# Kernel tuning notes

Hardware: AMD Instinct MI355X
Metric: run time of the kernel (lower is better)

Reference implementation:

```python
import jax, jax.numpy as jnp
import numpy as np

TOP_K = 2  # active_experts


def setup_inputs() -> dict:
    key = jax.random.key(0)
    k0, k1, k2, k3 = jax.random.split(key, 4)
    B, S, D, E, H = 4, 1024, 2048, 16, 1024
    x = jax.random.normal(k0, (B, S, D), jnp.float32) * 0.02
    Wg = jax.random.normal(k1, (E, D), jnp.float32) * 0.02          # gate: Linear(dim, E, bias=False)
    balance_bias = jnp.zeros((E,), jnp.float32)                      # registered buffer, init zeros
    W1 = jax.random.normal(k2, (E, D, H), jnp.float32) * 0.02        # expert up-proj (no bias)
    W2 = jax.random.normal(k3, (E, H, D), jnp.float32) * 0.02        # expert down-proj (no bias)
    return {"x": x, "Wg": Wg, "balance_bias": balance_bias, "W1": W1, "W2": W2}


def reference(x, Wg, balance_bias, W1, W2):
    B, S, D = x.shape
    E = Wg.shape[0]
    xf = x.reshape(-1, D)                                   # [T, D], T = B*S
    T = xf.shape[0]

    # sigmoid gating with load-balance bias
    gate_logits = xf @ Wg.T                                 # [T, E]
    gate_scores = jax.nn.sigmoid(gate_logits + balance_bias)

    # top-k selection + normalization (matches torch.topk + sum-normalize)
    topk_scores, topk_idx = jax.lax.top_k(gate_scores, TOP_K)
    topk_scores = topk_scores / (topk_scores.sum(-1, keepdims=True) + 1e-6)

    # dense combine weights [T, E]: zero for unselected experts -> identical math
    # to the per-expert masked index_add in the original module
    combine = jnp.zeros((T, E), xf.dtype).at[jnp.arange(T)[:, None], topk_idx].add(topk_scores)

    # per-expert FFN: SiLU(x W1_e) W2_e, weighted-combined across experts
    h = jax.nn.silu(jnp.einsum('td,edh->teh', xf, W1))      # [T, E, H]
    out = jnp.einsum('teh,te,ehd->td', h, combine, W2)      # [T, D]
    return out.reshape(B, S, D)
```

## Files before the change

### kernel.cpp

```cpp
#include <hip/hip_runtime.h>
#include <math.h>

#define T_TOK 4096
#define DDIM  2048
#define HDIM  1024
#define NEXP  16
#define CAP   4096
#define GBM   128
#define GBN   128
#define GBK   64
#define MAX_TILES 80

typedef __attribute__((ext_vector_type(8))) short  short8;
typedef __attribute__((ext_vector_type(4))) float  floatx4;

__device__ __forceinline__ unsigned short f2bf(float f) {
    unsigned int u = __float_as_uint(f);
    u += 0x7fffu + ((u >> 16) & 1u);
    return (unsigned short)(u >> 16);
}
__device__ __forceinline__ float bf2f(unsigned short u) {
    return __uint_as_float((unsigned int)u << 16);
}

__device__ __forceinline__ void gl_lds16(const void* g, void* l) {
    __builtin_amdgcn_global_load_lds(
        (const __attribute__((address_space(1))) unsigned int*)g,
        (__attribute__((address_space(3))) unsigned int*)l,
        16, 0, 0);
}

__global__ __launch_bounds__(256, 4) void prep_kernel(
    const float* __restrict__ x, const float* __restrict__ Wg,
    const float* __restrict__ bias,
    const float* __restrict__ W1, const float* __restrict__ W2,
    unsigned short* __restrict__ W1T, unsigned short* __restrict__ W2T,
    int* __restrict__ counts, int* __restrict__ tok_list,
    int4* __restrict__ tinfo, float2* __restrict__ wcomb,
    unsigned short* __restrict__ xbf)
{
    __shared__ __align__(16) unsigned short Ls[64 * 256];
    int z   = blockIdx.z;
    int bid = blockIdx.x;
    int tid = threadIdx.x;

    if (bid < 128) {
        const float* src; unsigned short* dst; int K, N, kt, nt;
        if (z < NEXP) {
            K = DDIM; N = HDIM;
            src = W1 + (size_t)z * K * N;
            dst = W1T + (size_t)z * (size_t)N * K;
            kt = bid >> 4; nt = bid & 15;
        } else {
            K = HDIM; N = DDIM;
            src = W2 + (size_t)(z - NEXP) * K * N;
            dst = W2T + (size_t)(z - NEXP) * (size_t)N * K;
            kt = bid >> 5; nt = bid & 31;
        }
        int kb = kt * 256, nb = nt * 64;
        int r = tid >> 4;
        int c16 = tid & 15;
        const float* s0 = src + (size_t)kb * N + nb + c16 * 4;

        float4 v[16];
#pragma unroll
        for (int i4 = 0; i4 < 4; ++i4)
#pragma unroll
            for (int i = 0; i < 4; ++i)
                v[i4 * 4 + i] = *(const float4*)(s0 + (size_t)(i4 * 64 + r * 4 + i) * N);

#pragma unroll
        for (int i4 = 0; i4 < 4; ++i4) {
#pragma unroll
            for (int j = 0; j < 4; ++j) {
                unsigned int lo = (unsigned int)f2bf(((const float*)&v[i4 * 4 + 0])[j])
                                | ((unsigned int)f2bf(((const float*)&v[i4 * 4 + 1])[j]) << 16);
                unsigned int hi = (unsigned int)f2bf(((const float*)&v[i4 * 4 + 2])[j])
                                | ((unsigned int)f2bf(((const float*)&v[i4 * 4 + 3])[j]) << 16);
                int n  = c16 * 4 + j;
                int g  = i4 * 16 + r;
                int gp = g ^ (n & 14);
                *(uint2*)&Ls[n * 256 + gp * 4] = make_uint2(lo, hi);
            }
        }
        __syncthreads();
        unsigned short* d0 = dst + (size_t)nb * K + kb;
#pragma unroll
        for (int j = 0; j < 8; ++j) {
            int c = tid + j * 256;
            int n = c >> 5, a = c & 31;
            int sp = (2 * a) ^ (n & 14);
            short8 sv = *(const short8*)&Ls[n * 256 + sp * 4];
            *(short8*)(d0 + (size_t)n * K + a * 8) = sv;
        }
        return;
    }

    int gb   = z * 8 + (bid - 128);
    int wv   = tid >> 6;
    int lane = tid & 63;
    const float4* wg4 = (const float4*)Wg;

    for (int tk = 0; tk < 4; ++tk) {
        int t = gb * 16 + wv * 4 + tk;

        const float4* xp4 = (const float4*)x + (size_t)t * (DDIM / 4);
        ushort4* xbp4 = (ushort4*)(xbf + (size_t)t * DDIM);

        float acc[NEXP];
#pragma unroll
        for (int e = 0; e < NEXP; ++e) acc[e] = 0.f;

        for (int it = 0; it < DDIM / 4 / 64; ++it) {
            int d4 = it * 64 + lane;
            float4 xv = xp4[d4];
            ushort4 xs;
            xs.x = f2bf(xv.x); xs.y = f2bf(xv.y);
            xs.z = f2bf(xv.z); xs.w = f2bf(xv.w);
            xbp4[d4] = xs;
#pragma unroll
            for (int e = 0; e < NEXP; ++e) {
                float4 wvv = wg4[e * (DDIM / 4) + d4];
                acc[e] += xv.x * wvv.x + xv.y * wvv.y + xv.z * wvv.z + xv.w * wvv.w;
            }
        }
#pragma unroll
        for (int e = 0; e < NEXP; ++e) {
            float v = acc[e];
#pragma unroll
            for (int off = 32; off > 0; off >>= 1) v += __shfl_xor(v, off, 64);
            acc[e] = v;
        }
        if (lane == 0) {
            float s[NEXP];
#pragma unroll
            for (int e = 0; e < NEXP; ++e)
                s[e] = 1.f / (1.f + expf(-(acc[e] + bias[e])));
            int i0 = 0;
#pragma unroll
            for (int e = 1; e < NEXP; ++e) if (s[e] > s[i0]) i0 = e;
            int i1 = (i0 == 0) ? 1 : 0;
            for (int e = 0; e < NEXP; ++e)
                if (e != i0 && s[e] > s[i1]) i1 = e;
            float denom = s[i0] + s[i1] + 1e-6f;
            int p0 = atomicAdd(&counts[i0], 1);
            tok_list[i0 * CAP + p0] = t;
            int p1 = atomicAdd(&counts[i1], 1);
            tok_list[i1 * CAP + p1] = t;
            tinfo[t] = make_int4(i0, p0, i1, p1);
            wcomb[t] = make_float2(s[i0] / denom, s[i1] / denom);
        }
    }
}

__global__ void scan_kernel(const int* __restrict__ counts, int* __restrict__ offsets,
                            int* __restrict__ ntiles, int* __restrict__ tile_e,
                            int* __restrict__ tile_mt)
{
    int lane = threadIdx.x;
    int c = (lane < NEXP) ? counts[lane] : 0;
    int incl = c;
#pragma unroll
    for (int d = 1; d < 64; d <<= 1) {
        int v = __shfl_up(incl, d, 64);
        if (lane >= d) incl += v;
    }
    if (lane < NEXP) offsets[lane] = incl - c;
    if (lane == NEXP - 1) offsets[NEXP] = incl;

    int nt_e = (lane < NEXP) ? ((c + GBM - 1) / GBM) : 0;
    int tincl = nt_e;
#pragma unroll
    for (int d = 1; d < 64; d <<= 1) {
        int v = __shfl_up(tincl, d, 64);
        if (lane >= d) tincl += v;
    }
    int tbase = tincl - nt_e;
    if (lane < NEXP) {
        for (int i = 0; i < nt_e; ++i) {
            tile_e[tbase + i]  = lane;
            tile_mt[tbase + i] = i;
        }
        if (lane == NEXP - 1) *ntiles = tbase + nt_e;
    }
}

__global__ __launch_bounds__(256) void up_gemm(
    const unsigned short* __restrict__ xbf, const unsigned short* __restrict__ W1T,
    const int* __restrict__ counts, const int* __restrict__ offsets,
    const int* __restrict__ ntiles, const int* __restrict__ tile_e,
    const int* __restrict__ tile_mt,
    const int* __restrict__ tok_list, unsigned short* __restrict__ hbuf)
{
    int idx = blockIdx.x;
    if (idx >= *ntiles) return;
    int e   = tile_e[idx];
    int mt  = tile_mt[idx];
    int cnt = counts[e];
    int nbase = blockIdx.y * GBN;

    __shared__ __align__(16) unsigned short As[2][GBM * GBK];
    __shared__ __align__(16) unsigned short Bs[2][GBN * GBK];

    int tid = threadIdx.x, lane = tid & 63, wv = tid >> 6;
    int kcL = ((lane & 7) ^ ((lane >> 3) & 7)) * 8;
    int hbase = offsets[e];

    const unsigned short* gA[4];
    const unsigned short* gB[4];
#pragma unroll
    for (int j = 0; j < 4; ++j) {
        int row = wv * 32 + j * 8 + (lane >> 3);
        int m = mt * GBM + row; if (m >= cnt) m = cnt - 1;
        int tok = tok_list[e * CAP + m];
        gA[j] = xbf + (size_t)tok * DDIM + kcL;
        gB[j] = W1T + ((size_t)e * HDIM + nbase + row) * DDIM + kcL;
    }
    int fr = lane & 15, fq = lane >> 4;
    int wm = (wv & 1) * 64, wn = (wv >> 1) * 64;

    floatx4 acc[4][4];
#pragma unroll
    for (int i = 0; i < 4; ++i)
#pragma unroll
        for (int j = 0; j < 4; ++j) acc[i][j] = (floatx4){0.f, 0.f, 0.f, 0.f};

#pragma unroll
    for (int j = 0; j < 4; ++j)
        gl_lds16(gA[j], &As[0][((wv * 4 + j) * 64 + lane) * 8]);
#pragma unroll
    for (int j = 0; j < 4; ++j)
        gl_lds16(gB[j], &Bs[0][((wv * 4 + j) * 64 + lane) * 8]);

    const int NK = DDIM / GBK;
    for (int i = 0; i < NK; ++i) {
        int cur = i & 1, nxt = cur ^ 1;
        __syncthreads();
        if (i + 1 < NK) {
            int k0 = (i + 1) * GBK;
#pragma unroll
            for (int j = 0; j < 4; ++j)
                gl_lds16(gA[j] + k0, &As[nxt][((wv * 4 + j) * 64 + lane) * 8]);
#pragma unroll
            for (int j = 0; j < 4; ++j)
                gl_lds16(gB[j] + k0, &Bs[nxt][((wv * 4 + j) * 64 + lane) * 8]);
        }
#pragma unroll
        for (int ks = 0; ks < 2; ++ks) {
            short8 af[4], bfr[4];
#pragma unroll
            for (int mi = 0; mi < 4; ++mi) {
                int row = wm + mi * 16 + fr;
                int kcs = (ks * 4 + fq) ^ (row & 7);
                af[mi] = *(const short8*)&As[cur][row * GBK + kcs * 8];
            }
#pragma unroll
            for (int ni = 0; ni < 4; ++ni) {
                int row = wn + ni * 16 + fr;
                int kcs = (ks * 4 + fq) ^ (row & 7);
                bfr[ni] = *(const short8*)&Bs[cur][row * GBK + kcs * 8];
            }
#pragma unroll
            for (int mi = 0; mi < 4; ++mi)
#pragma unroll
                for (int ni = 0; ni < 4; ++ni)
                    acc[mi][ni] = __builtin_amdgcn_mfma_f32_16x16x32_bf16(
                        af[mi], bfr[ni], acc[mi][ni], 0, 0, 0);
        }
    }

#pragma unroll
    for (int mi = 0; mi < 4; ++mi) {
#pragma unroll
        for (int r = 0; r < 4; ++r) {
            int row = wm + mi * 16 + fq * 4 + r;
            int m = mt * GBM + row;
            if (m < cnt) {
                size_t ro = (size_t)(hbase + m) * HDIM + nbase + wn;
#pragma unroll
                for (int ni = 0; ni < 4; ++ni) {
                    float u  = acc[mi][ni][r];
                    float hh = u / (1.f + __expf(-u));
                    hbuf[ro + ni * 16 + fr] = f2bf(hh);
                }
            }
        }
    }
}

__global__ __launch_bounds__(256) void down_gemm(
    const unsigned short* __restrict__ hbuf, const unsigned short* __restrict__ W2T,
    const int* __restrict__ counts, const int* __restrict__ offsets,
    const int* __restrict__ ntiles, const int* __restrict__ tile_e,
    const int* __restrict__ tile_mt,
    unsigned short* __restrict__ ybuf)
{
    int idx = blockIdx.x;
    if (idx >= *ntiles) return;
    int e   = tile_e[idx];
    int mt  = tile_mt[idx];
    int cnt = counts[e];
    int nbase = blockIdx.y * GBN;

    __shared__ __align__(16) unsigned short As[2][GBM * GBK];
    __shared__ __align__(16) unsigned short Bs[2][GBN * GBK];

    int tid = threadIdx.x, lane = tid & 63, wv = tid >> 6;
    int kcL = ((lane & 7) ^ ((lane >> 3) & 7)) * 8;
    int hbase = offsets[e];

    const unsigned short* gA[4];
    const unsigned short* gB[4];
#pragma unroll
    for (int j = 0; j < 4; ++j) {
        int row = wv * 32 + j * 8 + (lane >> 3);
        int m = mt * GBM + row; if (m >= cnt) m = cnt - 1;
        gA[j] = hbuf + (size_t)(hbase + m) * HDIM + kcL;
        gB[j] = W2T + ((size_t)e * DDIM + nbase + row) * HDIM + kcL;
    }
    int fr = lane & 15, fq = lane >> 4;
    int wm = (wv & 1) * 64, wn = (wv >> 1) * 64;

    floatx4 acc[4][4];
#pragma unroll
    for (int i = 0; i < 4; ++i)
#pragma unroll
        for (int j = 0; j < 4; ++j) acc[i][j] = (floatx4){0.f, 0.f, 0.f, 0.f};

#pragma unroll
    for (int j = 0; j < 4; ++j)
        gl_lds16(gA[j], &As[0][((wv * 4 + j) * 64 + lane) * 8]);
#pragma unroll
    for (int j = 0; j < 4; ++j)
        gl_lds16(gB[j], &Bs[0][((wv * 4 + j) * 64 + lane) * 8]);

    const int NK = HDIM / GBK;
    for (int i = 0; i < NK; ++i) {
        int cur = i & 1, nxt = cur ^ 1;
        __syncthreads();
        if (i + 1 < NK) {
            int k0 = (i + 1) * GBK;
#pragma unroll
            for (int j = 0; j < 4; ++j)
                gl_lds16(gA[j] + k0, &As[nxt][((wv * 4 + j) * 64 + lane) * 8]);
#pragma unroll
            for (int j = 0; j < 4; ++j)
                gl_lds16(gB[j] + k0, &Bs[nxt][((wv * 4 + j) * 64 + lane) * 8]);
        }
#pragma unroll
        for (int ks = 0; ks < 2; ++ks) {
            short8 af[4], bfr[4];
#pragma unroll
            for (int mi = 0; mi < 4; ++mi) {
                int row = wm + mi * 16 + fr;
                int kcs = (ks * 4 + fq) ^ (row & 7);
                af[mi] = *(const short8*)&As[cur][row * GBK + kcs * 8];
            }
#pragma unroll
            for (int ni = 0; ni < 4; ++ni) {
                int row = wn + ni * 16 + fr;
                int kcs = (ks * 4 + fq) ^ (row & 7);
                bfr[ni] = *(const short8*)&Bs[cur][row * GBK + kcs * 8];
            }
#pragma unroll
            for (int mi = 0; mi < 4; ++mi)
#pragma unroll
                for (int ni = 0; ni < 4; ++ni)
                    acc[mi][ni] = __builtin_amdgcn_mfma_f32_16x16x32_bf16(
                        af[mi], bfr[ni], acc[mi][ni], 0, 0, 0);
        }
    }

#pragma unroll
    for (int mi = 0; mi < 4; ++mi) {
#pragma unroll
        for (int r = 0; r < 4; ++r) {
            int row = wm + mi * 16 + fq * 4 + r;
            int m = mt * GBM + row;
            if (m < cnt) {
                size_t ro = (size_t)(hbase + m) * DDIM + nbase + wn;
#pragma unroll
                for (int ni = 0; ni < 4; ++ni)
                    ybuf[ro + ni * 16 + fr] = f2bf(acc[mi][ni][r]);
            }
        }
    }
}

__global__ __launch_bounds__(256) void combine_kernel(
    const unsigned short* __restrict__ ybuf, const int* __restrict__ offsets,
    const int4* __restrict__ tinfo, const float2* __restrict__ wcomb,
    float* __restrict__ out)
{
    int t = blockIdx.x;
    int4   ti = tinfo[t];
    float2 w  = wcomb[t];
    int s0 = offsets[ti.x] + ti.y;
    int s1 = offsets[ti.z] + ti.w;
    const ushort4* y0 = (const ushort4*)(ybuf + (size_t)s0 * DDIM);
    const ushort4* y1 = (const ushort4*)(ybuf + (size_t)s1 * DDIM);
    float4* op = (float4*)(out + (size_t)t * DDIM);
#pragma unroll
    for (int i = 0; i < 2; ++i) {
        int c = threadIdx.x + i * 256;
        ushort4 a = y0[c], b = y1[c];
        float4 r;
        r.x = w.x * bf2f(a.x) + w.y * bf2f(b.x);
        r.y = w.x * bf2f(a.y) + w.y * bf2f(b.y);
        r.z = w.x * bf2f(a.z) + w.y * bf2f(b.z);
        r.w = w.x * bf2f(a.w) + w.y * bf2f(b.w);
        op[c] = r;
    }
}

extern "C" void kernel_launch(void* const* d_in, const int* in_sizes, int n_in,
                              void* d_out, int out_size, void* d_ws, size_t ws_size,
                              hipStream_t stream)
{
    const float* x    = (const float*)d_in[0];
    const float* Wg   = (const float*)d_in[1];
    const float* bias = (const float*)d_in[2];
    const float* W1   = (const float*)d_in[3];
    const float* W2   = (const float*)d_in[4];
    float* out = (float*)d_out;

    char* ws = (char*)d_ws;
    int*            counts   = (int*)(ws + 0);
    int*            offsets  = (int*)(ws + 256);
    int*            ntiles   = (int*)(ws + 512);
    int*            tile_e   = (int*)(ws + 512 + 4);
    int*            tile_mt  = (int*)(ws + 512 + 4 + MAX_TILES * 4);
    int*            tok_list = (int*)(ws + 2048);
    int4*           tinfo    = (int4*)(ws + 264192);
    float2*         wcomb    = (float2*)(ws + 329728);
    unsigned short* xbf      = (unsigned short*)(ws + 524288);
    unsigned short* hbuf     = (unsigned short*)(ws + 17301504);
    unsigned short* ybuf     = (unsigned short*)(ws + 34078720);
    unsigned short* W1T      = (unsigned short*)(ws + 67633152);
    unsigned short* W2T      = (unsigned short*)(ws + 134742016);

    hipMemsetAsync(counts, 0, 64, stream);

    prep_kernel<<<dim3(136, 1, 32), 256, 0, stream>>>(
        x, Wg, bias, W1, W2, W1T, W2T, counts, tok_list, tinfo, wcomb, xbf);
    scan_kernel<<<1, 64, 0, stream>>>(counts, offsets, ntiles, tile_e, tile_mt);
    up_gemm<<<dim3(MAX_TILES, HDIM / GBN), 256, 0, stream>>>(
        xbf, W1T, counts, offsets, ntiles, tile_e, tile_mt, tok_list, hbuf);
    down_gemm<<<dim3(MAX_TILES, DDIM / GBN), 256, 0, stream>>>(
        hbuf, W2T, counts, offsets, ntiles, tile_e, tile_mt, ybuf);
    combine_kernel<<<T_TOK, 256, 0, stream>>>(ybuf, offsets, tinfo, wcomb, out);
}
```

Baseline: 652.6 us.

## Fuse fp32 weight conversion into expert GEMMs, drop separate transpose pass

Removes the prep pass that converted and transposed W1/W2 into bf16 scratch buffers. Each GEMM now loads fp32 weight tiles into registers, converts them to bf16 and writes them transposed and swizzled into LDS, overlapping the next tile's load with the MFMA loop. The gate computation becomes its own kernel with one token per wave. This saves a full weight write and re-read, but weights are now re-read in fp32 once per token tile, and the async global-to-LDS path is replaced by register staging.

```diff
diff --git a/kernel.cpp b/kernel.cpp
--- a/kernel.cpp
+++ b/kernel.cpp
@@ -30,126 +30,64 @@
         16, 0, 0);
 }
 
-__global__ __launch_bounds__(256, 4) void prep_kernel(
+__global__ __launch_bounds__(256) void gate_kernel(
     const float* __restrict__ x, const float* __restrict__ Wg,
     const float* __restrict__ bias,
-    const float* __restrict__ W1, const float* __restrict__ W2,
-    unsigned short* __restrict__ W1T, unsigned short* __restrict__ W2T,
     int* __restrict__ counts, int* __restrict__ tok_list,
     int4* __restrict__ tinfo, float2* __restrict__ wcomb,
     unsigned short* __restrict__ xbf)
 {
-    __shared__ __align__(16) unsigned short Ls[64 * 256];
-    int z   = blockIdx.z;
-    int bid = blockIdx.x;
-    int tid = threadIdx.x;
-
-    if (bid < 128) {
-        const float* src; unsigned short* dst; int K, N, kt, nt;
-        if (z < NEXP) {
-            K = DDIM; N = HDIM;
-            src = W1 + (size_t)z * K * N;
-            dst = W1T + (size_t)z * (size_t)N * K;
-            kt = bid >> 4; nt = bid & 15;
-        } else {
-            K = HDIM; N = DDIM;
-            src = W2 + (size_t)(z - NEXP) * K * N;
-            dst = W2T + (size_t)(z - NEXP) * (size_t)N * K;
-            kt = bid >> 5; nt = bid & 31;
-        }
-        int kb = kt * 256, nb = nt * 64;
-        int r = tid >> 4;
-        int c16 = tid & 15;
-        const float* s0 = src + (size_t)kb * N + nb + c16 * 4;
-
-        float4 v[16];
-#pragma unroll
-        for (int i4 = 0; i4 < 4; ++i4)
-#pragma unroll
-            for (int i = 0; i < 4; ++i)
-                v[i4 * 4 + i] = *(const float4*)(s0 + (size_t)(i4 * 64 + r * 4 + i) * N);
-
-#pragma unroll
-        for (int i4 = 0; i4 < 4; ++i4) {
-#pragma unroll
-            for (int j = 0; j < 4; ++j) {
-                unsigned int lo = (unsigned int)f2bf(((const float*)&v[i4 * 4 + 0])[j])
-                                | ((unsigned int)f2bf(((const float*)&v[i4 * 4 + 1])[j]) << 16);
-                unsigned int hi = (unsigned int)f2bf(((const float*)&v[i4 * 4 + 2])[j])
-                                | ((unsigned int)f2bf(((const float*)&v[i4 * 4 + 3])[j]) << 16);
-                int n  = c16 * 4 + j;
-                int g  = i4 * 16 + r;
-                int gp = g ^ (n & 14);
-                *(uint2*)&Ls[n * 256 + gp * 4] = make_uint2(lo, hi);
-            }
-        }
-        __syncthreads();
-        unsigned short* d0 = dst + (size_t)nb * K + kb;
-#pragma unroll
-        for (int j = 0; j < 8; ++j) {
-            int c = tid + j * 256;
-            int n = c >> 5, a = c & 31;
-            int sp = (2 * a) ^ (n & 14);
-            short8 sv = *(const short8*)&Ls[n * 256 + sp * 4];
-            *(short8*)(d0 + (size_t)n * K + a * 8) = sv;
-        }
-        return;
-    }
-
-    int gb   = z * 8 + (bid - 128);
-    int wv   = tid >> 6;
-    int lane = tid & 63;
+    int tb   = blockIdx.x;
+    int wv   = threadIdx.x >> 6;
+    int lane = threadIdx.x & 63;
+    int t    = tb * 4 + wv;
+
+    const float4* xp4 = (const float4*)x + (size_t)t * (DDIM / 4);
+    ushort4* xbp4 = (ushort4*)(xbf + (size_t)t * DDIM);
     const float4* wg4 = (const float4*)Wg;
 
-    for (int tk = 0; tk < 4; ++tk) {
-        int t = gb * 16 + wv * 4 + tk;
-
-        const float4* xp4 = (const float4*)x + (size_t)t * (DDIM / 4);
-        ushort4* xbp4 = (ushort4*)(xbf + (size_t)t * DDIM);
-
-        float acc[NEXP];
-#pragma unroll
-        for (int e = 0; e < NEXP; ++e) acc[e] = 0.f;
-
-        for (int it = 0; it < DDIM / 4 / 64; ++it) {
-            int d4 = it * 64 + lane;
-            float4 xv = xp4[d4];
-            ushort4 xs;
-            xs.x = f2bf(xv.x); xs.y = f2bf(xv.y);
-            xs.z = f2bf(xv.z); xs.w = f2bf(xv.w);
-            xbp4[d4] = xs;
-#pragma unroll
-            for (int e = 0; e < NEXP; ++e) {
-                float4 wvv = wg4[e * (DDIM / 4) + d4];
-                acc[e] += xv.x * wvv.x + xv.y * wvv.y + xv.z * wvv.z + xv.w * wvv.w;
-            }
-        }
+    float acc[NEXP];
+#pragma unroll
+    for (int e = 0; e < NEXP; ++e) acc[e] = 0.f;
+
+    for (int it = 0; it < DDIM / 4 / 64; ++it) {
+        int d4 = it * 64 + lane;
+        float4 xv = xp4[d4];
+        ushort4 xs;
+        xs.x = f2bf(xv.x); xs.y = f2bf(xv.y);
+        xs.z = f2bf(xv.z); xs.w = f2bf(xv.w);
+        xbp4[d4] = xs;
 #pragma unroll
         for (int e = 0; e < NEXP; ++e) {
-            float v = acc[e];
-#pragma unroll
-            for (int off = 32; off > 0; off >>= 1) v += __shfl_xor(v, off, 64);
-            acc[e] = v;
-        }
-        if (lane == 0) {
-            float s[NEXP];
-#pragma unroll
-            for (int e = 0; e < NEXP; ++e)
-                s[e] = 1.f / (1.f + expf(-(acc[e] + bias[e])));
-            int i0 = 0;
-#pragma unroll
-            for (int e = 1; e < NEXP; ++e) if (s[e] > s[i0]) i0 = e;
-            int i1 = (i0 == 0) ? 1 : 0;
-            for (int e = 0; e < NEXP; ++e)
-                if (e != i0 && s[e] > s[i1]) i1 = e;
-            float denom = s[i0] + s[i1] + 1e-6f;
-            int p0 = atomicAdd(&counts[i0], 1);
-            tok_list[i0 * CAP + p0] = t;
-            int p1 = atomicAdd(&counts[i1], 1);
-            tok_list[i1 * CAP + p1] = t;
-            tinfo[t] = make_int4(i0, p0, i1, p1);
-            wcomb[t] = make_float2(s[i0] / denom, s[i1] / denom);
-        }
+            float4 wvv = wg4[e * (DDIM / 4) + d4];
+            acc[e] += xv.x * wvv.x + xv.y * wvv.y + xv.z * wvv.z + xv.w * wvv.w;
+        }
+    }
+#pragma unroll
+    for (int e = 0; e < NEXP; ++e) {
+        float v = acc[e];
+#pragma unroll
+        for (int off = 32; off > 0; off >>= 1) v += __shfl_xor(v, off, 64);
+        acc[e] = v;
+    }
+    if (lane == 0) {
+        float s[NEXP];
+#pragma unroll
+        for (int e = 0; e < NEXP; ++e)
+            s[e] = 1.f / (1.f + expf(-(acc[e] + bias[e])));
+        int i0 = 0;
+#pragma unroll
+        for (int e = 1; e < NEXP; ++e) if (s[e] > s[i0]) i0 = e;
+        int i1 = (i0 == 0) ? 1 : 0;
+        for (int e = 0; e < NEXP; ++e)
+            if (e != i0 && s[e] > s[i1]) i1 = e;
+        float denom = s[i0] + s[i1] + 1e-6f;
+        int p0 = atomicAdd(&counts[i0], 1);
+        tok_list[i0 * CAP + p0] = t;
+        int p1 = atomicAdd(&counts[i1], 1);
+        tok_list[i1 * CAP + p1] = t;
+        tinfo[t] = make_int4(i0, p0, i1, p1);
+        wcomb[t] = make_float2(s[i0] / denom, s[i1] / denom);
     }
 }
 
@@ -185,8 +123,9 @@
     }
 }
 
+
 __global__ __launch_bounds__(256) void up_gemm(
-    const unsigned short* __restrict__ xbf, const unsigned short* __restrict__ W1T,
+    const unsigned short* __restrict__ xbf, const float* __restrict__ W1,
     const int* __restrict__ counts, const int* __restrict__ offsets,
     const int* __restrict__ ntiles, const int* __restrict__ tile_e,
     const int* __restrict__ tile_mt,
@@ -198,6 +137,7 @@
     int mt  = tile_mt[idx];
     int cnt = counts[e];
     int nbase = blockIdx.y * GBN;
+    const int N = HDIM;
 
     __shared__ __align__(16) unsigned short As[2][GBM * GBK];
     __shared__ __align__(16) unsigned short Bs[2][GBN * GBK];
@@ -207,15 +147,22 @@
     int hbase = offsets[e];
 
     const unsigned short* gA[4];
-    const unsigned short* gB[4];
 #pragma unroll
     for (int j = 0; j < 4; ++j) {
         int row = wv * 32 + j * 8 + (lane >> 3);
         int m = mt * GBM + row; if (m >= cnt) m = cnt - 1;
         int tok = tok_list[e * CAP + m];
         gA[j] = xbf + (size_t)tok * DDIM + kcL;
-        gB[j] = W1T + ((size_t)e * HDIM + nbase + row) * DDIM + kcL;
-    }
+    }
+
+    const float* wB = W1 + (size_t)e * DDIM * HDIM;
+    int ng = lane >> 2, kg = lane & 3;
+    int nh = (wv & 1) * 64, kh = (wv >> 1) * 32;
+    int nloc = nh + ng * 4;
+    const float* gBbase = wB + (size_t)(kh + kg * 4) * N + nbase + nloc;
+    int cbase = (kh >> 3) + (kg >> 1);
+    int koff  = (kg & 1) * 4;
+
     int fr = lane & 15, fq = lane >> 4;
     int wm = (wv & 1) * 64, wn = (wv >> 1) * 64;
 
@@ -225,12 +172,28 @@
 #pragma unroll
         for (int j = 0; j < 4; ++j) acc[i][j] = (floatx4){0.f, 0.f, 0.f, 0.f};
 
+    float4 bv[8];
 #pragma unroll
     for (int j = 0; j < 4; ++j)
         gl_lds16(gA[j], &As[0][((wv * 4 + j) * 64 + lane) * 8]);
 #pragma unroll
-    for (int j = 0; j < 4; ++j)
-        gl_lds16(gB[j], &Bs[0][((wv * 4 + j) * 64 + lane) * 8]);
+    for (int i4 = 0; i4 < 2; ++i4)
+#pragma unroll
+        for (int ld = 0; ld < 4; ++ld)
+            bv[i4 * 4 + ld] = *(const float4*)(gBbase + (size_t)(i4 * 16 + ld) * N);
+#pragma unroll
+    for (int i4 = 0; i4 < 2; ++i4) {
+#pragma unroll
+        for (int j = 0; j < 4; ++j) {
+            unsigned int lo = (unsigned int)f2bf(((const float*)&bv[i4 * 4 + 0])[j])
+                            | ((unsigned int)f2bf(((const float*)&bv[i4 * 4 + 1])[j]) << 16);
+            unsigned int hi = (unsigned int)f2bf(((const float*)&bv[i4 * 4 + 2])[j])
+                            | ((unsigned int)f2bf(((const float*)&bv[i4 * 4 + 3])[j]) << 16);
+            int row = nloc + j;
+            int gsl = (cbase + i4 * 2) ^ (((row >> 3) ^ row) & 7);
+            *(uint2*)&Bs[0][row * GBK + gsl * 8 + koff] = make_uint2(lo, hi);
+        }
+    }
 
     const int NK = DDIM / GBK;
     for (int i = 0; i < NK; ++i) {
@@ -242,8 +205,10 @@
             for (int j = 0; j < 4; ++j)
                 gl_lds16(gA[j] + k0, &As[nxt][((wv * 4 + j) * 64 + lane) * 8]);
 #pragma unroll
-            for (int j = 0; j < 4; ++j)
-                gl_lds16(gB[j] + k0, &Bs[nxt][((wv * 4 + j) * 64 + lane) * 8]);
+            for (int i4 = 0; i4 < 2; ++i4)
+#pragma unroll
+                for (int ld = 0; ld < 4; ++ld)
+                    bv[i4 * 4 + ld] = *(const float4*)(gBbase + (size_t)(k0 + i4 * 16 + ld) * N);
         }
 #pragma unroll
         for (int ks = 0; ks < 2; ++ks) {
@@ -257,7 +222,7 @@
 #pragma unroll
             for (int ni = 0; ni < 4; ++ni) {
                 int row = wn + ni * 16 + fr;
-                int kcs = (ks * 4 + fq) ^ (row & 7);
+                int kcs = (ks * 4 + fq) ^ (((row >> 3) ^ row) & 7);
                 bfr[ni] = *(const short8*)&Bs[cur][row * GBK + kcs * 8];
             }
 #pragma unroll
@@ -266,6 +231,21 @@
                 for (int ni = 0; ni < 4; ++ni)
                     acc[mi][ni] = __builtin_amdgcn_mfma_f32_16x16x32_bf16(
                         af[mi], bfr[ni], acc[mi][ni], 0, 0, 0);
+        }
+        if (i + 1 < NK) {
+#pragma unroll
+            for (int i4 = 0; i4 < 2; ++i4) {
+#pragma unroll
+                for (int j = 0; j < 4; ++j) {
+                    unsigned int lo = (unsigned int)f2bf(((const float*)&bv[i4 * 4 + 0])[j])
+                                    | ((unsigned int)f2bf(((const float*)&bv[i4 * 4 + 1])[j]) << 16);
+                    unsigned int hi = (unsigned int)f2bf(((const float*)&bv[i4 * 4 + 2])[j])
+                                    | ((unsigned int)f2bf(((const float*)&bv[i4 * 4 + 3])[j]) << 16);
+                    int row = nloc + j;
+                    int gsl = (cbase + i4 * 2) ^ (((row >> 3) ^ row) & 7);
+                    *(uint2*)&Bs[nxt][row * GBK + gsl * 8 + koff] = make_uint2(lo, hi);
+                }
+            }
         }
     }
 
@@ -289,7 +269,7 @@
 }
 
 __global__ __launch_bounds__(256) void down_gemm(
-    const unsigned short* __restrict__ hbuf, const unsigned short* __restrict__ W2T,
+    const unsigned short* __restrict__ hbuf, const float* __restrict__ W2,
     const int* __restrict__ counts, const int* __restrict__ offsets,
     const int* __restrict__ ntiles, const int* __restrict__ tile_e,
     const int* __restrict__ tile_mt,
@@ -301,6 +281,7 @@
     int mt  = tile_mt[idx];
     int cnt = counts[e];
     int nbase = blockIdx.y * GBN;
+    const int N = DDIM;
 
     __shared__ __align__(16) unsigned short As[2][GBM * GBK];
     __shared__ __align__(16) unsigned short Bs[2][GBN * GBK];
@@ -310,14 +291,21 @@
     int hbase = offsets[e];
 
     const unsigned short* gA[4];
-    const unsigned short* gB[4];
 #pragma unroll
     for (int j = 0; j < 4; ++j) {
         int row = wv * 32 + j * 8 + (lane >> 3);
         int m = mt * GBM + row; if (m >= cnt) m = cnt - 1;
         gA[j] = hbuf + (size_t)(hbase + m) * HDIM + kcL;
-        gB[j] = W2T + ((size_t)e * DDIM + nbase + row) * HDIM + kcL;
-    }
+    }
+
+    const float* wB = W2 + (size_t)e * HDIM * DDIM;
+    int ng = lane >> 2, kg = lane & 3;
+    int nh = (wv & 1) * 64, kh = (wv >> 1) * 32;
+    int nloc = nh + ng * 4;
+    const float* gBbase = wB + (size_t)(kh + kg * 4) * N + nbase + nloc;
+    int cbase = (kh >> 3) + (kg >> 1);
+    int koff  = (kg & 1) * 4;
+
     int fr = lane & 15, fq = lane >> 4;
     int wm = (wv & 1) * 64, wn = (wv >> 1) * 64;
 
@@ -327,12 +315,28 @@
 #pragma unroll
         for (int j = 0; j < 4; ++j) acc[i][j] = (floatx4){0.f, 0.f, 0.f, 0.f};
 
+    float4 bv[8];
 #pragma unroll
     for (int j = 0; j < 4; ++j)
         gl_lds16(gA[j], &As[0][((wv * 4 + j) * 64 + lane) * 8]);
 #pragma unroll
-    for (int j = 0; j < 4; ++j)
-        gl_lds16(gB[j], &Bs[0][((wv * 4 + j) * 64 + lane) * 8]);
+    for (int i4 = 0; i4 < 2; ++i4)
+#pragma unroll
+        for (int ld = 0; ld < 4; ++ld)
+            bv[i4 * 4 + ld] = *(const float4*)(gBbase + (size_t)(i4 * 16 + ld) * N);
+#pragma unroll
+    for (int i4 = 0; i4 < 2; ++i4) {
+#pragma unroll
+        for (int j = 0; j < 4; ++j) {
+            unsigned int lo = (unsigned int)f2bf(((const float*)&bv[i4 * 4 + 0])[j])
+                            | ((unsigned int)f2bf(((const float*)&bv[i4 * 4 + 1])[j]) << 16);
+            unsigned int hi = (unsigned int)f2bf(((const float*)&bv[i4 * 4 + 2])[j])
+                            | ((unsigned int)f2bf(((const float*)&bv[i4 * 4 + 3])[j]) << 16);
+            int row = nloc + j;
+            int gsl = (cbase + i4 * 2) ^ (((row >> 3) ^ row) & 7);
+            *(uint2*)&Bs[0][row * GBK + gsl * 8 + koff] = make_uint2(lo, hi);
+        }
+    }
 
     const int NK = HDIM / GBK;
     for (int i = 0; i < NK; ++i) {
@@ -344,8 +348,10 @@
             for (int j = 0; j < 4; ++j)
                 gl_lds16(gA[j] + k0, &As[nxt][((wv * 4 + j) * 64 + lane) * 8]);
 #pragma unroll
-            for (int j = 0; j < 4; ++j)
-                gl_lds16(gB[j] + k0, &Bs[nxt][((wv * 4 + j) * 64 + lane) * 8]);
+            for (int i4 = 0; i4 < 2; ++i4)
+#pragma unroll
+                for (int ld = 0; ld < 4; ++ld)
+                    bv[i4 * 4 + ld] = *(const float4*)(gBbase + (size_t)(k0 + i4 * 16 + ld) * N);
         }
 #pragma unroll
         for (int ks = 0; ks < 2; ++ks) {
@@ -359,7 +365,7 @@
 #pragma unroll
             for (int ni = 0; ni < 4; ++ni) {
                 int row = wn + ni * 16 + fr;
-                int kcs = (ks * 4 + fq) ^ (row & 7);
+                int kcs = (ks * 4 + fq) ^ (((row >> 3) ^ row) & 7);
                 bfr[ni] = *(const short8*)&Bs[cur][row * GBK + kcs * 8];
             }
 #pragma unroll
@@ -368,6 +374,21 @@
                 for (int ni = 0; ni < 4; ++ni)
                     acc[mi][ni] = __builtin_amdgcn_mfma_f32_16x16x32_bf16(
                         af[mi], bfr[ni], acc[mi][ni], 0, 0, 0);
+        }
+        if (i + 1 < NK) {
+#pragma unroll
+            for (int i4 = 0; i4 < 2; ++i4) {
+#pragma unroll
+                for (int j = 0; j < 4; ++j) {
+                    unsigned int lo = (unsigned int)f2bf(((const float*)&bv[i4 * 4 + 0])[j])
+                                    | ((unsigned int)f2bf(((const float*)&bv[i4 * 4 + 1])[j]) << 16);
+                    unsigned int hi = (unsigned int)f2bf(((const float*)&bv[i4 * 4 + 2])[j])
+                                    | ((unsigned int)f2bf(((const float*)&bv[i4 * 4 + 3])[j]) << 16);
+                    int row = nloc + j;
+                    int gsl = (cbase + i4 * 2) ^ (((row >> 3) ^ row) & 7);
+                    *(uint2*)&Bs[nxt][row * GBK + gsl * 8 + koff] = make_uint2(lo, hi);
+                }
+            }
         }
     }
 
@@ -436,17 +457,15 @@
     unsigned short* xbf      = (unsigned short*)(ws + 524288);
     unsigned short* hbuf     = (unsigned short*)(ws + 17301504);
     unsigned short* ybuf     = (unsigned short*)(ws + 34078720);
-    unsigned short* W1T      = (unsigned short*)(ws + 67633152);
-    unsigned short* W2T      = (unsigned short*)(ws + 134742016);
 
     hipMemsetAsync(counts, 0, 64, stream);
 
-    prep_kernel<<<dim3(136, 1, 32), 256, 0, stream>>>(
-        x, Wg, bias, W1, W2, W1T, W2T, counts, tok_list, tinfo, wcomb, xbf);
+    gate_kernel<<<dim3(T_TOK / 4), 256, 0, stream>>>(
+        x, Wg, bias, counts, tok_list, tinfo, wcomb, xbf);
     scan_kernel<<<1, 64, 0, stream>>>(counts, offsets, ntiles, tile_e, tile_mt);
     up_gemm<<<dim3(MAX_TILES, HDIM / GBN), 256, 0, stream>>>(
-        xbf, W1T, counts, offsets, ntiles, tile_e, tile_mt, tok_list, hbuf);
+        xbf, W1, counts, offsets, ntiles, tile_e, tile_mt, tok_list, hbuf);
     down_gemm<<<dim3(MAX_TILES, DDIM / GBN), 256, 0, stream>>>(
-        hbuf, W2T, counts, offsets, ntiles, tile_e, tile_mt, ybuf);
+        hbuf, W2, counts, offsets, ntiles, tile_e, tile_mt, ybuf);
     combine_kernel<<<T_TOK, 256, 0, stream>>>(ybuf, offsets, tinfo, wcomb, out);
 }
```

New measurement: 692.5 us. 1.06x slower.
